# Optimization experiments

Hardware: AMD Instinct MI355X
Metric: run time of the kernel (lower is better)

Reference implementation:

```python
import jax, jax.numpy as jnp
from jax import lax
import numpy as np

H = 48; W = 48; C_IN = 256; A_PER = 3
M = A_PER * H * W            # 6912 anchors
IMG = 768.0                  # square image, clip bound for x and y
OBJ_THR = 0.3; IOU_THR = 0.7; TOP_K = 2000
NEG = -1e9                   # finite sentinel for masked scores


def _make_anchors():
    stride = IMG / H
    base = 2.0 * stride
    ratios = np.array([0.5, 1.0, 2.0])
    ws = base * np.sqrt(ratios)          # [3]
    hs = base / np.sqrt(ratios)
    cx = (np.arange(W) + 0.5) * stride
    cy = (np.arange(H) + 0.5) * stride
    cxg, cyg = np.meshgrid(cx, cy)       # [H, W]
    anc = np.stack([
        cxg[None] - ws[:, None, None] / 2,
        cyg[None] - hs[:, None, None] / 2,
        cxg[None] + ws[:, None, None] / 2,
        cyg[None] + hs[:, None, None] / 2,
    ], axis=-1)                           # [3, H, W, 4] matches (anchor, h, w) flatten order
    return jnp.asarray(anc.reshape(-1, 4), jnp.float32)


def setup_inputs() -> dict:
    key = jax.random.key(0)
    ks = jax.random.split(key, 4)
    x = jax.random.normal(ks[0], (1, C_IN, H, W), jnp.float32)
    conv_w = jax.random.normal(ks[1], (256, 256, 3, 3), jnp.float32) * 0.02
    conv_b = jnp.zeros((256,), jnp.float32)
    det_w = jax.random.normal(ks[2], (3, 256, 1, 1), jnp.float32) * 0.02
    det_b = jnp.zeros((3,), jnp.float32)
    reg_w = jax.random.normal(ks[3], (12, 256, 1, 1), jnp.float32) * 0.02
    reg_b = jnp.zeros((12,), jnp.float32)
    anchors = _make_anchors()
    return {"x": x, "conv_w": conv_w, "conv_b": conv_b, "det_w": det_w,
            "det_b": det_b, "reg_w": reg_w, "reg_b": reg_b, "anchors": anchors}


def reference(x, conv_w, conv_b, det_w, det_b, reg_w, reg_b, anchors):
    # ---- FPN 3x3 conv + RPN head (1x1 convs) ----
    inter = lax.conv_general_dilated(
        x, conv_w, (1, 1), 'SAME',
        dimension_numbers=('NCHW', 'OIHW', 'NCHW')) + conv_b[None, :, None, None]
    obj = jax.nn.sigmoid(jnp.einsum('nchw,oc->nohw', inter, det_w[:, :, 0, 0])
                         + det_b[None, :, None, None])          # [1,3,H,W]
    reg = (jnp.einsum('nchw,oc->nohw', inter, reg_w[:, :, 0, 0])
           + reg_b[None, :, None, None])                        # [1,12,H,W]

    scores = obj.reshape(-1)                                    # [M], (anchor,h,w) order
    deltas = reg.reshape(1, 4, A_PER, H, W).transpose(0, 2, 3, 4, 1).reshape(-1, 4)

    # ---- box decode (preserves the source's cx/cy quirk: cx = y1 + w/2, cy = x1 + h/2) ----
    x1, y1, x2, y2 = anchors[:, 0], anchors[:, 1], anchors[:, 2], anchors[:, 3]
    aw = x2 - x1; ah = y2 - y1
    acx = y1 + aw / 2; acy = x1 + ah / 2
    dx, dy, dw, dh = deltas[:, 0], deltas[:, 1], deltas[:, 2], deltas[:, 3]
    px = acx + dx * aw; py = acy + dy * ah
    pw = aw * jnp.exp(dw); ph = ah * jnp.exp(dh)
    boxes = jnp.stack([px - pw / 2, py - ph / 2, px + pw / 2, py + ph / 2], axis=-1)

    # ---- clip to image ----
    boxes = jnp.clip(boxes, 0.0, IMG)

    # ---- validity: degenerate filter (source's naming quirk) + objectness threshold ----
    hts = boxes[:, 2] - boxes[:, 0]
    wds = boxes[:, 3] - boxes[:, 1]
    valid = (hts > 0) & (wds > 0) & (scores > OBJ_THR)

    # ---- greedy NMS (jit-friendly: sort, pairwise IoU, sequential suppression) ----
    s = jnp.where(valid, scores, NEG)
    order = jnp.argsort(-s)
    b = boxes[order]; v = valid[order]; ss = s[order]
    area = (b[:, 2] - b[:, 0]) * (b[:, 3] - b[:, 1])             # [M]
    iw = jnp.clip(jnp.minimum(b[:, None, 2], b[None, :, 2])
                  - jnp.maximum(b[:, None, 0], b[None, :, 0]), 0.0)
    ih = jnp.clip(jnp.minimum(b[:, None, 3], b[None, :, 3])
                  - jnp.maximum(b[:, None, 1], b[None, :, 1]), 0.0)
    inter_a = iw * ih                                             # [M,M]
    iou = inter_a / jnp.maximum(area[:, None] + area[None, :] - inter_a, 1e-9)

    idx = jnp.arange(M)

    def body(suppressed, i):
        keep_i = v[i] & (~suppressed[i])
        sup = keep_i & (iou[i] > IOU_THR) & (idx > i)
        return suppressed | sup, keep_i

    _, keeps = lax.scan(body, jnp.zeros(M, bool), idx)            # keep mask (sorted order)

    # ---- top-k proposal selection (fixed K, padded with sentinels) ----
    out_s = jnp.where(keeps, ss, NEG)
    topv, topi = lax.top_k(out_s, TOP_K)
    vtop = keeps[topi]
    out_scores = jnp.where(vtop, topv, -1.0)                      # [TOP_K]
    out_boxes = jnp.where(vtop[:, None], b[topi], 0.0)            # [TOP_K, 4]
    return out_scores, out_boxes
```

## Files before the change

### kernel.cpp

```cpp
#include <hip/hip_runtime.h>
#include <cstdint>

#define NPX 2304
#define MM 6912
#define NW 108
#define TOPK 2000
#define NEGV -1000000000.0f
#define OBJ_THRF 0.3f
#define IOU_THRF 0.7f
#define IMGF 768.0f

typedef unsigned long long u64;
typedef unsigned int u32;

__device__ __forceinline__ u64 shfl64(u64 v, int src) {
  int lo = __shfl((int)(v & 0xffffffffull), src, 64);
  int hi = __shfl((int)(v >> 32), src, 64);
  return ((u64)(u32)hi << 32) | (u32)lo;
}

__global__ __launch_bounds__(256) void k_conv(const float* __restrict__ x,
                                              const float* __restrict__ cw,
                                              float* __restrict__ interp) {
  __shared__ float xs[16 * 3 * 50];
  __shared__ float wl[144 * 66];
  const int tid = threadIdx.x;
  const int og = tid & 15;
  const int pg = tid >> 4;
  const int oc0 = blockIdx.x * 64;
  const int h = blockIdx.y;
  const int ks = blockIdx.z;

  float acc[4][3];
#pragma unroll
  for (int i = 0; i < 4; i++)
#pragma unroll
    for (int j = 0; j < 3; j++) acc[i][j] = 0.f;

  for (int icc = 0; icc < 8; ++icc) {
    const int ic0 = ks * 128 + icc * 16;
    for (int e = tid; e < 2400; e += 256) {
      int ic = e / 150, rem = e % 150;
      int r = rem / 50, col = rem % 50 - 1;
      int gr = h - 1 + r;
      float v = 0.f;
      if (col >= 0 && col < 48 && gr >= 0 && gr < 48)
        v = x[(ic0 + ic) * NPX + gr * 48 + col];
      xs[e] = v;
    }
    for (int e = tid; e < 9216; e += 256) {
      int oc = e / 144, it = e % 144;
      wl[it * 66 + oc] = cw[(oc0 + oc) * 2304 + ic0 * 9 + it];
    }
    __syncthreads();
#pragma unroll
    for (int ic = 0; ic < 16; ++ic) {
      float xr[3][5];
#pragma unroll
      for (int r = 0; r < 3; r++)
#pragma unroll
        for (int q = 0; q < 5; q++)
          xr[r][q] = xs[(ic * 3 + r) * 50 + 3 * pg + q];
#pragma unroll
      for (int r = 0; r < 3; r++)
#pragma unroll
        for (int dxk = 0; dxk < 3; dxk++) {
          int it = ic * 9 + r * 3 + dxk;
          const float2 w01 = *(const float2*)&wl[it * 66 + og * 4];
          const float2 w23 = *(const float2*)&wl[it * 66 + og * 4 + 2];
          float wv[4] = {w01.x, w01.y, w23.x, w23.y};
#pragma unroll
          for (int p = 0; p < 3; p++) {
            float xv = xr[r][p + dxk];
#pragma unroll
            for (int kk = 0; kk < 4; kk++) acc[kk][p] += wv[kk] * xv;
          }
        }
    }
    __syncthreads();
  }
#pragma unroll
  for (int kk = 0; kk < 4; kk++) {
    int oc = oc0 + og * 4 + kk;
#pragma unroll
    for (int p = 0; p < 3; p++)
      interp[ks * (256 * NPX) + oc * NPX + h * 48 + 3 * pg + p] = acc[kk][p];
  }
}

__global__ __launch_bounds__(256) void k_decode(const float* __restrict__ interp,
                                                const float* __restrict__ cb,
                                                const float* __restrict__ dw,
                                                const float* __restrict__ db,
                                                const float* __restrict__ rw,
                                                const float* __restrict__ rb,
                                                const float* __restrict__ anch,
                                                float* __restrict__ s,
                                                float4* __restrict__ boxes) {
  __shared__ float wl[256 * 16];
  const int tid = threadIdx.x;
  const int p = blockIdx.x * 256 + tid;
  for (int e = tid; e < 3840; e += 256) {
    int o = e % 15, c = e / 15;
    wl[c * 16 + o] = (o < 3) ? dw[o * 256 + c] : rw[(o - 3) * 256 + c];
  }
  __syncthreads();
  float acc[15];
#pragma unroll
  for (int o = 0; o < 15; o++) acc[o] = 0.f;
  const float* p0 = interp;
  const float* p1 = interp + 256 * NPX;
  for (int c = 0; c < 256; ++c) {
    float v = p0[c * NPX + p] + p1[c * NPX + p] + cb[c];
#pragma unroll
    for (int o = 0; o < 15; o++) acc[o] += v * wl[c * 16 + o];
  }
  const float4* an4 = (const float4*)anch;
#pragma unroll
  for (int a = 0; a < 3; ++a) {
    int m = a * NPX + p;
    float logit = acc[a] + db[a];
    float score = 1.f / (1.f + expf(-logit));
    float dxv = acc[3 + 0 + a] + rb[0 + a];
    float dyv = acc[3 + 3 + a] + rb[3 + a];
    float dwv = acc[3 + 6 + a] + rb[6 + a];
    float dhv = acc[3 + 9 + a] + rb[9 + a];
    float4 an = an4[m];
    float aw = an.z - an.x;
    float ah = an.w - an.y;
    float acx = an.y + aw * 0.5f;
    float acy = an.x + ah * 0.5f;
    float pxc = acx + dxv * aw;
    float pyc = acy + dyv * ah;
    float pw = aw * expf(dwv);
    float ph = ah * expf(dhv);
    float b0 = pxc - pw * 0.5f, b1 = pyc - ph * 0.5f;
    float b2 = pxc + pw * 0.5f, b3 = pyc + ph * 0.5f;
    b0 = fminf(fmaxf(b0, 0.f), IMGF);
    b1 = fminf(fmaxf(b1, 0.f), IMGF);
    b2 = fminf(fmaxf(b2, 0.f), IMGF);
    b3 = fminf(fmaxf(b3, 0.f), IMGF);
    float hts = b2 - b0, wds = b3 - b1;
    bool valid = (hts > 0.f) && (wds > 0.f) && (score > OBJ_THRF);
    s[m] = valid ? score : NEGV;
    boxes[m] = make_float4(b0, b1, b2, b3);
  }
}

__global__ __launch_bounds__(256) void k_sortA(const float* __restrict__ s,
                                               u64* __restrict__ keys) {
  __shared__ u64 lds[1024];
  const int tid = threadIdx.x;
  const int b = blockIdx.x;
  for (int v = tid; v < 1024; v += 256) {
    int i = b * 1024 + v;
    u64 p;
    if (i < MM) {
      u32 u = __float_as_uint(s[i]);
      u = u ^ (u32)(((int)u >> 31) | 0x80000000);
      p = ((u64)(~u) << 32) | (u32)i;
    } else {
      p = ~0ull;
    }
    lds[v] = p;
  }
  for (u32 kk = 2; kk <= 1024; kk <<= 1) {
    for (u32 j = kk >> 1; j > 0; j >>= 1) {
      __syncthreads();
#pragma unroll 2
      for (int t = tid; t < 512; t += 256) {
        int i = ((t & ~(j - 1)) << 1) | (t & (j - 1));
        int l = i | j;
        bool up = ((i & kk) == 0);
        u64 a = lds[i], c = lds[l];
        u64 mn = a < c ? a : c;
        u64 mx = a < c ? c : a;
        lds[i] = up ? mn : mx;
        lds[l] = up ? mx : mn;
      }
    }
  }
  __syncthreads();
  for (int v = tid; v < 1024; v += 256) keys[b * 1024 + v] = lds[v];
}

__global__ __launch_bounds__(256) void k_merge(const u64* __restrict__ in,
                                               u64* __restrict__ outk, int L, int fin,
                                               const float* __restrict__ s,
                                               const float4* __restrict__ boxes,
                                               float* __restrict__ ssc,
                                               float4* __restrict__ sboxes) {
  const int i = blockIdx.x * 256 + threadIdx.x;
  const int pair = i / (2 * L);
  const int r = i - pair * 2 * L;
  const u64* A = in + (size_t)pair * 2 * L;
  const u64* B = A + L;
  int lo = (r > L) ? (r - L) : 0;
  int hi = (r < L) ? r : L;
  while (lo < hi) {
    int mid = (lo + hi) >> 1;
    if (A[mid] < B[r - 1 - mid]) lo = mid + 1; else hi = mid;
  }
  int a = lo, bi = r - lo;
  u64 av = (a < L) ? A[a] : ~0ull;
  u64 bv = (bi < L) ? B[bi] : ~0ull;
  u64 o = (av < bv) ? av : bv;
  outk[i] = o;
  if (fin && i < MM) {
    int idx = (int)(u32)o;
    ssc[i] = s[idx];
    sboxes[i] = boxes[idx];
  }
}

__global__ __launch_bounds__(256) void k_zero(u64* __restrict__ nz) {
  int i = blockIdx.x * 256 + threadIdx.x;
  if (i < MM * 2) nz[i] = 0;
}

__global__ __launch_bounds__(256) void k_mask(const float4* __restrict__ sboxes,
                                              u64* __restrict__ mask_t,
                                              u64* __restrict__ nz) {
  __shared__ float4 rb_[64];
  const int rt = blockIdx.x;
  const int w = blockIdx.y * 4 + (threadIdx.x >> 6);
  const int lane = threadIdx.x & 63;
  if (threadIdx.x < 64) rb_[threadIdx.x] = sboxes[rt * 64 + threadIdx.x];
  __syncthreads();
  if (w < rt) return;
  float4 c = sboxes[w * 64 + lane];
  float areaC = (c.z - c.x) * (c.w - c.y);
  u64 myw = 0;
  for (int r = 0; r < 64; ++r) {
    float4 b = rb_[r];
    float iw = fmaxf(fminf(b.z, c.z) - fmaxf(b.x, c.x), 0.f);
    float ih = fmaxf(fminf(b.w, c.w) - fmaxf(b.y, c.y), 0.f);
    float inter = iw * ih;
    float areaB = (b.z - b.x) * (b.w - b.y);
    float un = fmaxf(areaB + areaC - inter, 1e-9f);
    bool bit = (inter / un) > IOU_THRF;
    u64 bal = __ballot(bit);
    if (lane == r) myw = bal;
  }
  mask_t[(size_t)w * MM + rt * 64 + lane] = myw;
  if (myw) atomicOr(&nz[(rt * 64 + lane) * 2 + (w >> 6)], 1ull << (w & 63));
}

__global__ __launch_bounds__(256) void k_scan(const u64* __restrict__ mask_t,
                                              const u64* __restrict__ nz,
                                              const float* __restrict__ ssc,
                                              const float4* __restrict__ sboxes,
                                              float* __restrict__ out) {
  __shared__ u64 remv[NW];
  __shared__ u64 keepw[NW];
  __shared__ int blist[64];
  __shared__ int nkS;
  __shared__ int kcntS;
  __shared__ int pref[NW];
  const int tid = threadIdx.x;
  if (tid < NW) { remv[tid] = 0; keepw[tid] = 0; }
  if (tid == 0) kcntS = 0;
  __syncthreads();

  for (int c = 0; c < NW; ++c) {
    if (tid < 64) {
      const int lane = tid;
      u64 dg = mask_t[(size_t)c * MM + c * 64 + lane];
      float sv = ssc[c * 64 + lane];
      u64 vb = __ballot(sv > OBJ_THRF);
      u64 w0 = remv[c];
      u64 cand = vb & ~w0;
      u64 above = (lane < 63) ? ~((2ull << lane) - 1ull) : 0ull;
      bool inC = ((cand >> lane) & 1ull) != 0;
      u64 conf = __ballot(inC && ((dg & above & cand) != 0ull));
      u64 kb;
      if (conf == 0ull) {
        kb = cand;
      } else {
        u64 w = w0;
        kb = 0;
        u64 rem = cand;
        while (rem) {
          int b = __ffsll(rem) - 1;
          kb |= (1ull << b);
          w |= shfl64(dg, b);
          rem = vb & ~w;
        }
      }
      int below = __popcll(kb & ((1ull << lane) - 1ull));
      if ((kb >> lane) & 1ull) blist[below] = lane;
      if (lane == 0) {
        keepw[c] = kb;
        nkS = __popcll(kb);
        kcntS += __popcll(kb);
      }
    }
    __syncthreads();
    int nk = nkS;
    if (tid < nk) {
      int row = c * 64 + blist[tid];
      u64 nz0 = nz[row * 2], nz1 = nz[row * 2 + 1];
      if (c < 64) {
        nz0 &= (c < 63) ? ~((2ull << c) - 1ull) : 0ull;
      } else {
        nz0 = 0;
        int cc = c - 64;
        nz1 &= ~((2ull << cc) - 1ull);
      }
      while (nz0) {
        int wv = __ffsll(nz0) - 1; nz0 &= nz0 - 1;
        atomicOr(&remv[wv], mask_t[(size_t)wv * MM + row]);
      }
      while (nz1) {
        int wv = __ffsll(nz1) - 1; nz1 &= nz1 - 1;
        atomicOr(&remv[wv + 64], mask_t[(size_t)(wv + 64) * MM + row]);
      }
    }
    __syncthreads();
    if (kcntS >= TOPK) break;
  }

  if (tid == 0) {
    int run = 0;
    for (int cc = 0; cc < NW; ++cc) { pref[cc] = run; run += __popcll(keepw[cc]); }
  }
  __syncthreads();
  for (int e = tid; e < TOPK * 5; e += 256) out[e] = (e < TOPK) ? -1.0f : 0.0f;
  __syncthreads();
  float4* ob = (float4*)(out + TOPK);
  for (int i = tid; i < MM; i += 256) {
    int cc = i >> 6, b = i & 63;
    u64 kb = keepw[cc];
    if ((kb >> b) & 1ull) {
      int rank = pref[cc] + __popcll(kb & ((1ull << b) - 1ull));
      if (rank < TOPK) {
        out[rank] = ssc[i];
        ob[rank] = sboxes[i];
      }
    }
  }
}

extern "C" void kernel_launch(void* const* d_in, const int* in_sizes, int n_in,
                              void* d_out, int out_size, void* d_ws, size_t ws_size,
                              hipStream_t stream) {
  const float* x  = (const float*)d_in[0];
  const float* cw = (const float*)d_in[1];
  const float* cb = (const float*)d_in[2];
  const float* dw = (const float*)d_in[3];
  const float* db = (const float*)d_in[4];
  const float* rw = (const float*)d_in[5];
  const float* rb = (const float*)d_in[6];
  const float* an = (const float*)d_in[7];
  char* ws = (char*)d_ws;
  float*  interp = (float*)(ws);
  u64*    keysA  = (u64*)(ws);
  u64*    keysB  = (u64*)(ws + 65536);
  float*  s      = (float*)(ws + 4718592);
  float4* boxes  = (float4*)(ws + 4746240);
  float*  ssc    = (float*)(ws + 4856832);
  float4* sboxes = (float4*)(ws + 4884480);
  u64*    mask   = (u64*)(ws + 4995072);
  u64*    nz     = (u64*)(ws + 10967040);
  float* out = (float*)d_out;

  hipLaunchKernelGGL(k_conv, dim3(4, 48, 2), dim3(256), 0, stream, x, cw, interp);
  hipLaunchKernelGGL(k_decode, dim3(9), dim3(256), 0, stream, interp, cb, dw, db, rw, rb, an, s, boxes);
  hipLaunchKernelGGL(k_zero, dim3(54), dim3(256), 0, stream, nz);
  hipLaunchKernelGGL(k_sortA, dim3(8), dim3(256), 0, stream, s, keysA);
  hipLaunchKernelGGL(k_merge, dim3(32), dim3(256), 0, stream, keysA, keysB, 1024, 0, s, boxes, ssc, sboxes);
  hipLaunchKernelGGL(k_merge, dim3(32), dim3(256), 0, stream, keysB, keysA, 2048, 0, s, boxes, ssc, sboxes);
  hipLaunchKernelGGL(k_merge, dim3(32), dim3(256), 0, stream, keysA, keysB, 4096, 1, s, boxes, ssc, sboxes);
  hipLaunchKernelGGL(k_mask, dim3(108, 27), dim3(256), 0, stream, sboxes, mask, nz);
  hipLaunchKernelGGL(k_scan, dim3(1), dim3(256), 0, stream, mask, nz, ssc, sboxes, out);
}
```

Before: 315.7 us.

## Restructure 3x3 conv: pre-transposed weights, pixel-per-thread tiling, 4-way K split

Adds a kernel that transposes conv weights to [ic*9][oc] layout. The conv is rewritten so each thread owns one pixel and 16 output channels, with 8 input rows staged in shared memory, and weights read as wave-uniform (broadcast) global loads instead of being staged in LDS. The input-channel split goes from 2 to 4, so the grid grows to 576 blocks for better occupancy, and decode now sums four partial buffers. The workspace layout is reorganised to make room for the transposed weights and the larger partial buffers, at the cost of an extra launch and more partial-sum traffic.

Result: slower. 332.6 us (+5.4%).

```diff
diff --git a/kernel.cpp b/kernel.cpp
--- a/kernel.cpp
+++ b/kernel.cpp
@@ -9,6 +9,7 @@
 #define OBJ_THRF 0.3f
 #define IOU_THRF 0.7f
 #define IMGF 768.0f
+#define KSPLIT 4
 
 typedef unsigned long long u64;
 typedef unsigned int u32;
@@ -19,76 +20,77 @@
   return ((u64)(u32)hi << 32) | (u32)lo;
 }
 
+__global__ __launch_bounds__(256) void k_wt(const float* __restrict__ cw,
+                                            float* __restrict__ wt) {
+  __shared__ float t[64][65];
+  const int it0 = blockIdx.x * 64;
+  const int oc0 = blockIdx.y * 64;
+  const int tx = threadIdx.x & 63;
+  const int ty = threadIdx.x >> 6;
+#pragma unroll
+  for (int k = 0; k < 16; ++k) {
+    int oc = ty + k * 4;
+    t[oc][tx] = cw[(oc0 + oc) * 2304 + it0 + tx];
+  }
+  __syncthreads();
+#pragma unroll
+  for (int k = 0; k < 16; ++k) {
+    int it = ty + k * 4;
+    wt[(it0 + it) * 256 + oc0 + tx] = t[tx][it];
+  }
+}
+
 __global__ __launch_bounds__(256) void k_conv(const float* __restrict__ x,
-                                              const float* __restrict__ cw,
-                                              float* __restrict__ interp) {
-  __shared__ float xs[16 * 3 * 50];
-  __shared__ float wl[144 * 66];
+                                              const float* __restrict__ wt,
+                                              float* __restrict__ part) {
+  __shared__ float xs[16 * 8 * 52];
   const int tid = threadIdx.x;
-  const int og = tid & 15;
-  const int pg = tid >> 4;
-  const int oc0 = blockIdx.x * 64;
-  const int h = blockIdx.y;
+  const int px = blockIdx.x * 256 + tid;
+  const int oc0 = blockIdx.y * 16;
   const int ks = blockIdx.z;
-
-  float acc[4][3];
-#pragma unroll
-  for (int i = 0; i < 4; i++)
-#pragma unroll
-    for (int j = 0; j < 3; j++) acc[i][j] = 0.f;
-
-  for (int icc = 0; icc < 8; ++icc) {
-    const int ic0 = ks * 128 + icc * 16;
-    for (int e = tid; e < 2400; e += 256) {
-      int ic = e / 150, rem = e % 150;
-      int r = rem / 50, col = rem % 50 - 1;
-      int gr = h - 1 + r;
+  const int row = px / 48, col = px % 48;
+  const int r0 = (blockIdx.x * 256) / 48;
+  const int rbase = row - r0;
+
+  float acc[16];
+#pragma unroll
+  for (int k = 0; k < 16; ++k) acc[k] = 0.f;
+
+  for (int icc = 0; icc < 64 / 16; ++icc) {
+    const int ic0 = ks * 64 + icc * 16;
+    for (int e = tid; e < 16 * 8 * 50; e += 256) {
+      int ic = e / 400, rem = e % 400;
+      int r = rem / 50, c = rem % 50 - 1;
+      int gr = r0 - 1 + r;
       float v = 0.f;
-      if (col >= 0 && col < 48 && gr >= 0 && gr < 48)
-        v = x[(ic0 + ic) * NPX + gr * 48 + col];
-      xs[e] = v;
-    }
-    for (int e = tid; e < 9216; e += 256) {
-      int oc = e / 144, it = e % 144;
-      wl[it * 66 + oc] = cw[(oc0 + oc) * 2304 + ic0 * 9 + it];
+      if (c >= 0 && c < 48 && gr >= 0 && gr < 48)
+        v = x[(ic0 + ic) * NPX + gr * 48 + c];
+      xs[(ic * 8 + r) * 52 + (c + 1)] = v;
     }
     __syncthreads();
-#pragma unroll
     for (int ic = 0; ic < 16; ++ic) {
-      float xr[3][5];
-#pragma unroll
-      for (int r = 0; r < 3; r++)
-#pragma unroll
-        for (int q = 0; q < 5; q++)
-          xr[r][q] = xs[(ic * 3 + r) * 50 + 3 * pg + q];
-#pragma unroll
-      for (int r = 0; r < 3; r++)
-#pragma unroll
-        for (int dxk = 0; dxk < 3; dxk++) {
-          int it = ic * 9 + r * 3 + dxk;
-          const float2 w01 = *(const float2*)&wl[it * 66 + og * 4];
-          const float2 w23 = *(const float2*)&wl[it * 66 + og * 4 + 2];
-          float wv[4] = {w01.x, w01.y, w23.x, w23.y};
-#pragma unroll
-          for (int p = 0; p < 3; p++) {
-            float xv = xr[r][p + dxk];
-#pragma unroll
-            for (int kk = 0; kk < 4; kk++) acc[kk][p] += wv[kk] * xv;
-          }
-        }
+      float xv[9];
+#pragma unroll
+      for (int dr = 0; dr < 3; ++dr)
+#pragma unroll
+        for (int dc = 0; dc < 3; ++dc)
+          xv[dr * 3 + dc] = xs[(ic * 8 + rbase + dr) * 52 + col + dc];
+      const float* wrow = wt + (size_t)(ic0 + ic) * 9 * 256 + oc0;
+#pragma unroll
+      for (int t = 0; t < 9; ++t) {
+        const float* wp = wrow + t * 256;
+#pragma unroll
+        for (int k = 0; k < 16; ++k) acc[k] += xv[t] * wp[k];
+      }
     }
     __syncthreads();
   }
 #pragma unroll
-  for (int kk = 0; kk < 4; kk++) {
-    int oc = oc0 + og * 4 + kk;
-#pragma unroll
-    for (int p = 0; p < 3; p++)
-      interp[ks * (256 * NPX) + oc * NPX + h * 48 + 3 * pg + p] = acc[kk][p];
-  }
-}
-
-__global__ __launch_bounds__(256) void k_decode(const float* __restrict__ interp,
+  for (int k = 0; k < 16; ++k)
+    part[((size_t)ks * 256 + oc0 + k) * NPX + px] = acc[k];
+}
+
+__global__ __launch_bounds__(256) void k_decode(const float* __restrict__ part,
                                                 const float* __restrict__ cb,
                                                 const float* __restrict__ dw,
                                                 const float* __restrict__ db,
@@ -108,10 +110,11 @@
   float acc[15];
 #pragma unroll
   for (int o = 0; o < 15; o++) acc[o] = 0.f;
-  const float* p0 = interp;
-  const float* p1 = interp + 256 * NPX;
   for (int c = 0; c < 256; ++c) {
-    float v = p0[c * NPX + p] + p1[c * NPX + p] + cb[c];
+    float v = cb[c];
+#pragma unroll
+    for (int kks = 0; kks < KSPLIT; ++kks)
+      v += part[((size_t)kks * 256 + c) * NPX + p];
 #pragma unroll
     for (int o = 0; o < 15; o++) acc[o] += v * wl[c * 16 + o];
   }
@@ -353,19 +356,21 @@
   const float* rb = (const float*)d_in[6];
   const float* an = (const float*)d_in[7];
   char* ws = (char*)d_ws;
-  float*  interp = (float*)(ws);
+  float*  part   = (float*)(ws);
   u64*    keysA  = (u64*)(ws);
   u64*    keysB  = (u64*)(ws + 65536);
-  float*  s      = (float*)(ws + 4718592);
-  float4* boxes  = (float4*)(ws + 4746240);
-  float*  ssc    = (float*)(ws + 4856832);
-  float4* sboxes = (float4*)(ws + 4884480);
-  u64*    mask   = (u64*)(ws + 4995072);
-  u64*    nz     = (u64*)(ws + 10967040);
+  u64*    mask   = (u64*)(ws);
+  u64*    nz     = (u64*)(ws + 5971968);
+  float*  wt     = (float*)(ws + 9437184);
+  float*  s      = (float*)(ws + 11796480);
+  float4* boxes  = (float4*)(ws + 11824128);
+  float*  ssc    = (float*)(ws + 11934720);
+  float4* sboxes = (float4*)(ws + 11962368);
   float* out = (float*)d_out;
 
-  hipLaunchKernelGGL(k_conv, dim3(4, 48, 2), dim3(256), 0, stream, x, cw, interp);
-  hipLaunchKernelGGL(k_decode, dim3(9), dim3(256), 0, stream, interp, cb, dw, db, rw, rb, an, s, boxes);
+  hipLaunchKernelGGL(k_wt, dim3(36, 4), dim3(256), 0, stream, cw, wt);
+  hipLaunchKernelGGL(k_conv, dim3(9, 16, KSPLIT), dim3(256), 0, stream, x, wt, part);
+  hipLaunchKernelGGL(k_decode, dim3(9), dim3(256), 0, stream, part, cb, dw, db, rw, rb, an, s, boxes);
   hipLaunchKernelGGL(k_zero, dim3(54), dim3(256), 0, stream, nz);
   hipLaunchKernelGGL(k_sortA, dim3(8), dim3(256), 0, stream, s, keysA);
   hipLaunchKernelGGL(k_merge, dim3(32), dim3(256), 0, stream, keysA, keysB, 1024, 0, s, boxes, ssc, sboxes);
```
